# Kernel tuning notes

Hardware: AMD Instinct MI355X
Metric: run time of the kernel (lower is better)

Reference implementation:

```python
import jax, jax.numpy as jnp
import numpy as np

X = 2048      # hidden units per layer
Z = 4         # number of hidden layers
IN = 512      # input_dim
OUT = 256     # output_dim
B = 64        # batch
T = 128       # time steps
KEEP = 0.7    # Bernoulli keep prob y
RES = [0, 0, 1, 2]  # residual_in (first two unused by the branch structure)
NFUN = 5      # number of candidate transfer functions


def setup_inputs() -> dict:
    key = jax.random.key(0)
    ks = jax.random.split(key, 12)
    f32 = jnp.float32
    x = jax.random.normal(ks[0], (B, T, IN), f32)
    W_in = jax.random.normal(ks[1], (X, IN), f32) * jax.random.bernoulli(ks[2], KEEP, (X, IN)).astype(f32)
    b_in = jax.random.normal(ks[3], (X,), f32)
    W_h = jax.random.normal(ks[4], (Z, X, 2 * X), f32)
    # lateral inhibition block: hidden layer 1, second-half columns, zero diagonal
    lat = jax.random.normal(ks[5], (X, X), f32) * (1.0 - jnp.eye(X, dtype=f32))
    W_h = W_h.at[1, :, X:].set(lat)
    W_h = W_h * jax.random.bernoulli(ks[6], KEEP, (Z, X, 2 * X)).astype(f32)
    b_h = jax.random.normal(ks[7], (Z, X), f32)
    W_out = jax.random.normal(ks[8], (OUT, X), f32) * jax.random.bernoulli(ks[9], KEEP, (OUT, X)).astype(f32)
    b_out = jax.random.normal(ks[10], (OUT,), f32)
    act_ids = jax.random.randint(ks[11], (Z + 1, X), 0, NFUN)
    out_act_ids = jax.random.randint(jax.random.fold_in(key, 99), (OUT,), 0, NFUN)
    return dict(x=x, W_in=W_in, b_in=b_in, W_h=W_h, b_h=b_h,
                W_out=W_out, b_out=b_out, act_ids=act_ids, out_act_ids=out_act_ids)


def _rand_act(h, ids):
    # per-column random nonlinearity: ids [D] in {relu, sigmoid, tanh, leaky_relu(0.1), selu}
    stk = jnp.stack([
        jax.nn.relu(h),
        jax.nn.sigmoid(h),
        jnp.tanh(h),
        jnp.where(h >= 0, h, 0.1 * h),
        jax.nn.selu(h),
    ], axis=0)  # [5, B, D]
    oh = jax.nn.one_hot(ids, NFUN, dtype=h.dtype)  # [D, 5]
    return jnp.einsum('fbd,df->bd', stk, oh)


def _l2norm(v, eps=1e-12):
    # torch F.normalize along dim=1
    return v / jnp.maximum(jnp.linalg.norm(v, axis=1, keepdims=True), eps)


def reference(x, W_in, b_in, W_h, b_h, W_out, b_out, act_ids, out_act_ids):
    batch = x.shape[0]

    def step(carry, xt):
        bp, li = carry  # backprojection state, lateral inhibition state
        h0 = _rand_act(xt @ W_in.T + b_in, act_ids[0])
        h1 = _rand_act(jnp.concatenate([h0, bp], axis=-1) @ W_h[0].T + b_h[0], act_ids[1])
        h2 = _rand_act(jnp.concatenate([h1, li], axis=-1) @ W_h[1].T + b_h[1], act_ids[2])
        li_new = _l2norm(h2)
        outs = [h0, h1, h2]
        for i in range(2, Z):
            hin = jnp.concatenate([outs[i], outs[RES[i]]], axis=-1)
            outs.append(_rand_act(hin @ W_h[i].T + b_h[i], act_ids[i + 1]))
        bp_new = _l2norm(outs[-1])
        yt = _rand_act(outs[-1] @ W_out.T + b_out, out_act_ids)
        return (bp_new, li_new), yt

    init = (jnp.zeros((batch, X), x.dtype), jnp.zeros((batch, X), x.dtype))
    _, ys = jax.lax.scan(step, init, jnp.swapaxes(x, 0, 1))  # scan over time
    return jnp.swapaxes(ys, 0, 1)  # [B, T, OUT]
```

## Files before the change

### kernel.cpp

```cpp
#include <hip/hip_runtime.h>
#include <stdint.h>


typedef __bf16 bf16;
typedef __attribute__((ext_vector_type(8))) __bf16 bf16x8;
typedef __attribute__((ext_vector_type(4))) float f32x4;

#define BATCH 64
#define TSTEPS 128
#define INDIM 512
#define XDIM 2048
#define OUTDIM 256
#define SLOTE ((size_t)BATCH * XDIM)
#define NBLOCKS 256
#define GSTRIDE 64
#define PBPAR ((size_t)3 * BATCH * XDIM)

__device__ __forceinline__ float apply_act(float h, int id) {
  switch (id) {
    case 0: return fmaxf(h, 0.0f);
    case 1: return 1.0f / (1.0f + __expf(-h));
    case 2: return tanhf(h);
    case 3: return h >= 0.0f ? h : 0.1f * h;
    default: {
      const float sc = 1.0507009873554805f;
      const float al = 1.6732632423543772f;
      return h > 0.0f ? sc * h : sc * al * (__expf(h) - 1.0f);
    }
  }
}

__device__ __forceinline__ bf16x8 cload(const bf16* p) {
  union { unsigned long long q[2]; bf16x8 v; } u;
  const unsigned long long* qp = (const unsigned long long*)p;
  u.q[0] = __hip_atomic_load(qp, __ATOMIC_RELAXED, __HIP_MEMORY_SCOPE_AGENT);
  u.q[1] = __hip_atomic_load(qp + 1, __ATOMIC_RELAXED, __HIP_MEMORY_SCOPE_AGENT);
  return u.v;
}

__device__ __forceinline__ void cstore8(unsigned long long* p,
                                        unsigned long long v) {
  unsigned long long old = __hip_atomic_exchange(p, v, __ATOMIC_RELAXED,
                                                 __HIP_MEMORY_SCOPE_AGENT);
  asm volatile("" :: "v"(old));
}

__device__ __forceinline__ unsigned long long cload8(
    const unsigned long long* p) {
  return __hip_atomic_load(p, __ATOMIC_RELAXED, __HIP_MEMORY_SCOPE_AGENT);
}

__device__ __forceinline__ void phase_wait(unsigned* bars, int bid,
                                           unsigned ph) {
  if (threadIdx.x == 0) {
    unsigned* done = bars + (size_t)8 * GSTRIDE;
    unsigned* rel = bars + (size_t)(9 + (bid >> 5)) * GSTRIDE;
    if ((bid & 31) == 0) {
      while (__hip_atomic_load(done, __ATOMIC_RELAXED,
                               __HIP_MEMORY_SCOPE_AGENT) < 64u * ph) {
        __builtin_amdgcn_s_sleep(2);
      }
      __hip_atomic_fetch_add(rel, 1u, __ATOMIC_RELAXED,
                             __HIP_MEMORY_SCOPE_AGENT);
    } else {
      while (__hip_atomic_load(rel, __ATOMIC_RELAXED,
                               __HIP_MEMORY_SCOPE_AGENT) < ph) {
        __builtin_amdgcn_s_sleep(2);
      }
    }
  }
  __syncthreads();
}

template <bool SCALE_A2, bool EMIT_SS, bool PLAIN_A1>
__device__ __forceinline__ void layer_phase(
    const int tid, const int nt, const int kq,
    const bf16* __restrict__ A1, const bf16* __restrict__ A2,
    const bf16x8 (&wf)[2][4], const float* __restrict__ bias,
    const int* __restrict__ acts, const float* __restrict__ ss_in,
    float* __restrict__ ss_out, bf16* __restrict__ outb,
    float* __restrict__ pbuf, unsigned* __restrict__ flags,
    unsigned* __restrict__ bars, const unsigned ph,
    float (&red)[8][64][33]) {
  const int lane = tid & 63;
  const int w = tid >> 6;
  const int l15 = lane & 15;
  const int kb8 = (lane >> 4) * 8;
  const int q4 = lane >> 4;

  const bf16* As = (kq >= 2) ? A2 : A1;
  const int koff = (kq & 1) * 1024 + w * 128;
  const bf16* ap = As + (size_t)l15 * 2048 + koff + kb8;

  f32x4 acc[4][2];
  const f32x4 zero = {0.f, 0.f, 0.f, 0.f};
#pragma unroll
  for (int mt = 0; mt < 4; mt++) {
    acc[mt][0] = zero;
    acc[mt][1] = zero;
  }

  const bool plain = PLAIN_A1 && (kq < 2);
#pragma unroll
  for (int ks = 0; ks < 4; ks++) {
#pragma unroll
    for (int mt = 0; mt < 4; mt++) {
      const bf16* aptr = ap + (size_t)mt * 16 * 2048 + ks * 32;
      bf16x8 a = plain ? *(const bf16x8*)aptr : cload(aptr);
      acc[mt][0] = __builtin_amdgcn_mfma_f32_16x16x32_bf16(a, wf[0][ks], acc[mt][0], 0, 0, 0);
      acc[mt][1] = __builtin_amdgcn_mfma_f32_16x16x32_bf16(a, wf[1][ks], acc[mt][1], 0, 0, 0);
    }
  }

#pragma unroll
  for (int mt = 0; mt < 4; mt++)
#pragma unroll
    for (int n2 = 0; n2 < 2; n2++)
#pragma unroll
      for (int r = 0; r < 4; r++)
        red[w][mt * 16 + q4 * 4 + r][n2 * 16 + l15] = acc[mt][n2][r];
  __syncthreads();

  const int row = tid >> 3;
  const int c4 = (tid & 7) * 4;
  float v[4];
#pragma unroll
  for (int j = 0; j < 4; j++) {
    float s = 0.f;
#pragma unroll
    for (int ww = 0; ww < 8; ww++) s += red[ww][row][c4 + j];
    v[j] = s;
  }

  float* pbase = pbuf + (size_t)(ph & 1) * PBPAR;
  const size_t pidx = ((size_t)row) * XDIM + nt * 32 + c4;
  if (kq != 0) {
    float* pb = pbase + (size_t)(kq - 1) * BATCH * XDIM + pidx;
    union { float f[2]; unsigned long long u; } pk;
    pk.f[0] = v[0]; pk.f[1] = v[1];
    cstore8((unsigned long long*)pb, pk.u);
    pk.f[0] = v[2]; pk.f[1] = v[3];
    cstore8((unsigned long long*)(pb + 2), pk.u);
    __syncthreads();
    if (tid == 0) {
      __hip_atomic_fetch_add(flags + (size_t)nt * GSTRIDE, 1u,
                             __ATOMIC_RELAXED, __HIP_MEMORY_SCOPE_AGENT);
    }
  } else {
    if (tid == 0) {
      while (__hip_atomic_load(flags + (size_t)nt * GSTRIDE, __ATOMIC_RELAXED,
                               __HIP_MEMORY_SCOPE_AGENT) < 3u * ph) {
        __builtin_amdgcn_s_sleep(1);
      }
    }
    __syncthreads();
    float p1[4], p2[4], p3[4];
#pragma unroll
    for (int h = 0; h < 2; h++) {
      union { unsigned long long u; float f[2]; } u1, u2, u3;
      const unsigned long long* b1 =
          (const unsigned long long*)(pbase + pidx) + h;
      u1.u = cload8(b1);
      u2.u = cload8(b1 + (size_t)BATCH * XDIM / 2);
      u3.u = cload8(b1 + (size_t)BATCH * XDIM);
      p1[h * 2] = u1.f[0]; p1[h * 2 + 1] = u1.f[1];
      p2[h * 2] = u2.f[0]; p2[h * 2 + 1] = u2.f[1];
      p3[h * 2] = u3.f[0]; p3[h * 2 + 1] = u3.f[1];
    }
    float scale = 1.0f;
    if (SCALE_A2) {
      float ssv = __hip_atomic_load(ss_in + row, __ATOMIC_RELAXED,
                                    __HIP_MEMORY_SCOPE_AGENT);
      scale = 1.0f / fmaxf(sqrtf(ssv), 1e-12f);
    }
    const int cg = nt * 32 + c4;
    union { bf16 b[4]; unsigned long long u; } hk;
    float ssl = 0.f;
#pragma unroll
    for (int j = 0; j < 4; j++) {
      float lo = v[j] + p1[j];
      float hi = p2[j] + p3[j];
      float pre = (SCALE_A2 ? (lo + scale * hi) : (lo + hi)) + bias[cg + j];
      float av = apply_act(pre, acts[cg + j]);
      hk.b[j] = (bf16)av;
      ssl += av * av;
    }
    if (EMIT_SS) {
      ssl += __shfl_xor(ssl, 1);
      ssl += __shfl_xor(ssl, 2);
      ssl += __shfl_xor(ssl, 4);
      if ((tid & 7) == 0) atomicAdd(ss_out + row, ssl);
    }
    cstore8((unsigned long long*)(outb + (size_t)row * XDIM + cg), hk.u);
    __syncthreads();
    if (tid == 0) {
      __hip_atomic_fetch_add(bars + (size_t)8 * GSTRIDE, 1u, __ATOMIC_RELAXED,
                             __HIP_MEMORY_SCOPE_AGENT);
    }
  }
}

struct StepParams {
  bf16* h0;
  bf16* extra;
  bf16* h1;
  bf16* h2a;
  bf16* h2b;
  bf16* h3;
  const bf16* whb;
  const float* b_h;
  const int* acts;
  float* ss_li;
  float* ss_bp;
  float* pbuf;
  unsigned* flags;
  unsigned* bar;
};

__global__ __launch_bounds__(512, 2) void step_loop(StepParams p) {
  __shared__ float red[8][64][33];
  const int tid = threadIdx.x;
  const int bid = blockIdx.x;
  const int nt = bid & 63;
  const int kq = bid >> 6;
  const int lane = tid & 63;
  const int w = tid >> 6;
  const int l15 = lane & 15;
  const int kb8 = (lane >> 4) * 8;
  const size_t wstr = (size_t)XDIM * 2 * XDIM;

  const bf16* wb = p.whb + (size_t)(nt * 32 + l15) * 4096 + kq * 1024 +
                   w * 128 + kb8;
  bf16x8 wf0[2][4], wf1[2][4], wf2[2][4], wf3[2][4];
#pragma unroll
  for (int n2 = 0; n2 < 2; n2++) {
#pragma unroll
    for (int ks = 0; ks < 4; ks++) {
      const bf16* q = wb + (size_t)n2 * 16 * 4096 + ks * 32;
      wf0[n2][ks] = *(const bf16x8*)q;
      wf1[n2][ks] = *(const bf16x8*)(q + wstr);
      wf2[n2][ks] = *(const bf16x8*)(q + 2 * wstr);
      wf3[n2][ks] = *(const bf16x8*)(q + 3 * wstr);
    }
  }

  unsigned ph = 0;
  for (int t = 0; t < TSTEPS; t++) {
#pragma unroll
    for (int n2 = 0; n2 < 2; n2++)
#pragma unroll
      for (int ks = 0; ks < 4; ks++) {
        asm volatile("" : "+v"(wf0[n2][ks]), "+v"(wf1[n2][ks]),
                          "+v"(wf2[n2][ks]), "+v"(wf3[n2][ks]));
      }

    const bf16* h4t = (t < 2) ? p.extra + (size_t)t * SLOTE
                              : p.h0 + (size_t)(t - 2) * SLOTE;
    bf16* h4n = (t + 1 < 2) ? p.extra + (size_t)(t + 1) * SLOTE
                            : p.h0 + (size_t)(t - 1) * SLOTE;
    bf16* h2n = (t & 1) ? p.h2b : p.h2a;
    const bf16* h2o = (t & 1) ? p.h2a : p.h2b;

    ++ph;
    layer_phase<true, false, true>(tid, nt, kq, p.h0 + (size_t)t * SLOTE, h4t,
                                   wf0, p.b_h, p.acts + XDIM,
                                   p.ss_bp + t * BATCH, nullptr, p.h1,
                                   p.pbuf, p.flags, p.bar, ph, red);
    phase_wait(p.bar, bid, ph);

    ++ph;
    layer_phase<true, true, false>(tid, nt, kq, p.h1, h2o, wf1, p.b_h + XDIM,
                                   p.acts + 2 * XDIM, p.ss_li + t * BATCH,
                                   p.ss_li + (t + 1) * BATCH, h2n,
                                   p.pbuf, p.flags, p.bar, ph, red);
    phase_wait(p.bar, bid, ph);

    ++ph;
    layer_phase<false, false, false>(tid, nt, kq, h2n, p.h1, wf2,
                                     p.b_h + 2 * XDIM, p.acts + 3 * XDIM,
                                     nullptr, nullptr, p.h3,
                                     p.pbuf, p.flags, p.bar, ph, red);
    phase_wait(p.bar, bid, ph);

    ++ph;
    layer_phase<false, true, false>(tid, nt, kq, p.h3, h2n, wf3,
                                    p.b_h + 3 * XDIM, p.acts + 4 * XDIM,
                                    nullptr, p.ss_bp + (t + 1) * BATCH, h4n,
                                    p.pbuf, p.flags, p.bar, ph, red);
    phase_wait(p.bar, bid, ph);
  }
}

__global__ __launch_bounds__(256) void h0_gemm(
    const bf16* __restrict__ A, const bf16* __restrict__ W,
    const float* __restrict__ bias, const int* __restrict__ acts,
    bf16* __restrict__ outp) {
  const int tid = threadIdx.x;
  const int lane = tid & 63;
  const int wv = tid >> 6;
  const int wm = (wv & 1) * 32;
  const int wn = (wv >> 1) * 64;
  const int nblk = blockIdx.x * 128;
  const int mblk = blockIdx.y * 64;
  const int l15 = lane & 15;
  const int kb8 = (lane >> 4) * 8;

  f32x4 acc[2][4];
  const f32x4 zero = {0.f, 0.f, 0.f, 0.f};
#pragma unroll
  for (int i = 0; i < 2; i++)
#pragma unroll
    for (int j = 0; j < 4; j++) acc[i][j] = zero;

  for (int kt = 0; kt < INDIM; kt += 32) {
    bf16x8 a[2], b[4];
#pragma unroll
    for (int mt = 0; mt < 2; mt++) {
      int m = mblk + wm + mt * 16 + l15;
      a[mt] = *(const bf16x8*)(A + (size_t)m * INDIM + kt + kb8);
    }
#pragma unroll
    for (int nt = 0; nt < 4; nt++) {
      int n = nblk + wn + nt * 16 + l15;
      b[nt] = *(const bf16x8*)(W + (size_t)n * INDIM + kt + kb8);
    }
#pragma unroll
    for (int mt = 0; mt < 2; mt++)
#pragma unroll
      for (int nt = 0; nt < 4; nt++)
        acc[mt][nt] = __builtin_amdgcn_mfma_f32_16x16x32_bf16(a[mt], b[nt], acc[mt][nt], 0, 0, 0);
  }

#pragma unroll
  for (int mt = 0; mt < 2; mt++) {
#pragma unroll
    for (int nt = 0; nt < 4; nt++) {
      int n = nblk + wn + nt * 16 + l15;
      float bv = bias[n];
      int aid = acts[n];
#pragma unroll
      for (int rr = 0; rr < 4; rr++) {
        int m = wm + mt * 16 + (lane >> 4) * 4 + rr;
        float v = apply_act(acc[mt][nt][rr] + bv, aid);
        int rowg = mblk + m;
        int bb = rowg >> 7;
        int tt = rowg & 127;
        outp[((size_t)tt * BATCH + bb) * XDIM + n] = (bf16)v;
      }
    }
  }
}

__global__ __launch_bounds__(256) void ybat_gemm(
    const bf16* __restrict__ extra, const bf16* __restrict__ h0,
    const bf16* __restrict__ Wout, const float* __restrict__ bout,
    const int* __restrict__ oact, float* __restrict__ out) {
  const int t = blockIdx.y;
  const int s = t + 1;
  const bf16* A = (s < 2) ? (extra + (size_t)s * SLOTE)
                          : (h0 + (size_t)(s - 2) * SLOTE);
  const int tid = threadIdx.x;
  const int lane = tid & 63;
  const int wv = tid >> 6;
  const int wm = (wv & 1) * 32;
  const int wn = (wv >> 1) * 64;
  const int nblk = blockIdx.x * 128;
  const int l15 = lane & 15;
  const int kb8 = (lane >> 4) * 8;

  f32x4 acc[2][4];
  const f32x4 zero = {0.f, 0.f, 0.f, 0.f};
#pragma unroll
  for (int i = 0; i < 2; i++)
#pragma unroll
    for (int j = 0; j < 4; j++) acc[i][j] = zero;

  for (int kt = 0; kt < XDIM; kt += 32) {
    bf16x8 a[2], b[4];
#pragma unroll
    for (int mt = 0; mt < 2; mt++) {
      int m = wm + mt * 16 + l15;
      a[mt] = *(const bf16x8*)(A + (size_t)m * XDIM + kt + kb8);
    }
#pragma unroll
    for (int nt = 0; nt < 4; nt++) {
      int n = nblk + wn + nt * 16 + l15;
      b[nt] = *(const bf16x8*)(Wout + (size_t)n * XDIM + kt + kb8);
    }
#pragma unroll
    for (int mt = 0; mt < 2; mt++)
#pragma unroll
      for (int nt = 0; nt < 4; nt++)
        acc[mt][nt] = __builtin_amdgcn_mfma_f32_16x16x32_bf16(a[mt], b[nt], acc[mt][nt], 0, 0, 0);
  }

#pragma unroll
  for (int mt = 0; mt < 2; mt++) {
#pragma unroll
    for (int nt = 0; nt < 4; nt++) {
      int n = nblk + wn + nt * 16 + l15;
      float bv = bout[n];
      int aid = oact[n];
#pragma unroll
      for (int rr = 0; rr < 4; rr++) {
        int b = wm + mt * 16 + (lane >> 4) * 4 + rr;
        float v = apply_act(acc[mt][nt][rr] + bv, aid);
        out[((size_t)b * TSTEPS + t) * OUTDIM + n] = v;
      }
    }
  }
}

__global__ __launch_bounds__(256) void cvt_bf16(
    const float* __restrict__ in, bf16* __restrict__ out, int n4) {
  int i = blockIdx.x * 256 + threadIdx.x;
  if (i < n4) {
    float4 v = ((const float4*)in)[i];
    union { bf16 b[4]; unsigned long long u; } pk;
    pk.b[0] = (bf16)v.x;
    pk.b[1] = (bf16)v.y;
    pk.b[2] = (bf16)v.z;
    pk.b[3] = (bf16)v.w;
    ((unsigned long long*)out)[i] = pk.u;
  }
}

__global__ __launch_bounds__(256) void zero32(uint32_t* __restrict__ p, int n) {
  int i = blockIdx.x * 256 + threadIdx.x;
  if (i < n) p[i] = 0u;
}

extern "C" void kernel_launch(void* const* d_in, const int* in_sizes, int n_in,
                              void* d_out, int out_size, void* d_ws, size_t ws_size,
                              hipStream_t stream) {
  const float* x     = (const float*)d_in[0];
  const float* W_in  = (const float*)d_in[1];
  const float* b_in  = (const float*)d_in[2];
  const float* W_h   = (const float*)d_in[3];
  const float* b_h   = (const float*)d_in[4];
  const float* W_out = (const float*)d_in[5];
  const float* b_out = (const float*)d_in[6];
  const int* act_ids = (const int*)d_in[7];
  const int* out_act = (const int*)d_in[8];
  float* out = (float*)d_out;

  char* w = (char*)d_ws;
  bf16* xbf   = (bf16*)w; w += (size_t)BATCH * TSTEPS * INDIM * 2;
  bf16* winb  = (bf16*)w; w += (size_t)XDIM * INDIM * 2;
  bf16* whb   = (bf16*)w; w += (size_t)4 * XDIM * (2 * XDIM) * 2;
  bf16* woutb = (bf16*)w; w += (size_t)OUTDIM * XDIM * 2;
  bf16* h0    = (bf16*)w; w += (size_t)TSTEPS * SLOTE * 2;
  bf16* h1    = (bf16*)w; w += SLOTE * 2;
  bf16* h3    = (bf16*)w; w += SLOTE * 2;
  float* pbuf = (float*)w; w += (size_t)2 * PBPAR * 4;
  char* zstart = w;
  bf16* extra = (bf16*)w; w += 2 * SLOTE * 2;
  bf16* h2a   = (bf16*)w; w += SLOTE * 2;
  bf16* h2b   = (bf16*)w; w += SLOTE * 2;
  float* ss_li = (float*)w; w += (size_t)(TSTEPS + 1) * BATCH * 4;
  float* ss_bp = (float*)w; w += (size_t)(TSTEPS + 1) * BATCH * 4;
  unsigned* flags = (unsigned*)w; w += (size_t)64 * GSTRIDE * 4;
  unsigned* bar = (unsigned*)w; w += (size_t)32 * GSTRIDE * 4;
  int zero_u32 = (int)((w - zstart) / 4);

  cvt_bf16<<<4096, 256, 0, stream>>>(x, xbf, (BATCH * TSTEPS * INDIM) / 4);
  cvt_bf16<<<1024, 256, 0, stream>>>(W_in, winb, (XDIM * INDIM) / 4);
  cvt_bf16<<<32768, 256, 0, stream>>>(W_h, whb, (4 * XDIM * 2 * XDIM) / 4);
  cvt_bf16<<<512, 256, 0, stream>>>(W_out, woutb, (OUTDIM * XDIM) / 4);
  zero32<<<(zero_u32 + 255) / 256, 256, 0, stream>>>((uint32_t*)zstart, zero_u32);
  h0_gemm<<<dim3(16, 128), 256, 0, stream>>>(xbf, winb, b_in, act_ids, h0);

  StepParams sp;
  sp.h0 = h0;
  sp.extra = extra;
  sp.h1 = h1;
  sp.h2a = h2a;
  sp.h2b = h2b;
  sp.h3 = h3;
  sp.whb = whb;
  sp.b_h = b_h;
  sp.acts = act_ids;
  sp.ss_li = ss_li;
  sp.ss_bp = ss_bp;
  sp.pbuf = pbuf;
  sp.flags = flags;
  sp.bar = bar;
  void* kp[] = {&sp};
  (void)hipLaunchCooperativeKernel((const void*)step_loop, dim3(NBLOCKS),
                                   dim3(512), kp, 0, stream);

  ybat_gemm<<<dim3(2, TSTEPS), 256, 0, stream>>>(
      extra, h0, woutb, b_out, out_act, out);
}
```

Before: 8.597 ms.

## Relax grid barrier so residual-half blocks start before previous layer finishes

Moves the grid barrier from after each layer to before it, and lets blocks whose K-quarter reads only the second (older) input start one phase early, since that input was produced two phases back. Split-K completion flags become per-quarter counters instead of one shared atomic. The block-to-tile mapping is reordered so the four K-quarters of an output tile are adjacent block ids. This aims to cut barrier stall and atomic contention, at the cost of subtler ordering: it depends on the early-start blocks not reading or overwriting data still in use, including partial buffers that alternate by phase parity.

```diff
diff --git a/kernel.cpp b/kernel.cpp
--- a/kernel.cpp
+++ b/kernel.cpp
@@ -50,21 +50,21 @@
   return __hip_atomic_load(p, __ATOMIC_RELAXED, __HIP_MEMORY_SCOPE_AGENT);
 }
 
-__device__ __forceinline__ void phase_wait(unsigned* bars, int bid,
-                                           unsigned ph) {
+__device__ __forceinline__ void start_wait(unsigned* bars, int bid,
+                                           unsigned tgt) {
   if (threadIdx.x == 0) {
     unsigned* done = bars + (size_t)8 * GSTRIDE;
     unsigned* rel = bars + (size_t)(9 + (bid >> 5)) * GSTRIDE;
     if ((bid & 31) == 0) {
       while (__hip_atomic_load(done, __ATOMIC_RELAXED,
-                               __HIP_MEMORY_SCOPE_AGENT) < 64u * ph) {
+                               __HIP_MEMORY_SCOPE_AGENT) < 64u * (tgt - 1u)) {
         __builtin_amdgcn_s_sleep(2);
       }
       __hip_atomic_fetch_add(rel, 1u, __ATOMIC_RELAXED,
                              __HIP_MEMORY_SCOPE_AGENT);
     } else {
       while (__hip_atomic_load(rel, __ATOMIC_RELAXED,
-                               __HIP_MEMORY_SCOPE_AGENT) < ph) {
+                               __HIP_MEMORY_SCOPE_AGENT) < tgt) {
         __builtin_amdgcn_s_sleep(2);
       }
     }
@@ -143,13 +143,22 @@
     cstore8((unsigned long long*)(pb + 2), pk.u);
     __syncthreads();
     if (tid == 0) {
-      __hip_atomic_fetch_add(flags + (size_t)nt * GSTRIDE, 1u,
+      __hip_atomic_fetch_add(flags + (size_t)nt * GSTRIDE + kq, 1u,
                              __ATOMIC_RELAXED, __HIP_MEMORY_SCOPE_AGENT);
     }
   } else {
     if (tid == 0) {
-      while (__hip_atomic_load(flags + (size_t)nt * GSTRIDE, __ATOMIC_RELAXED,
-                               __HIP_MEMORY_SCOPE_AGENT) < 3u * ph) {
+      unsigned* f = flags + (size_t)nt * GSTRIDE;
+      while (__hip_atomic_load(f + 1, __ATOMIC_RELAXED,
+                               __HIP_MEMORY_SCOPE_AGENT) < ph) {
+        __builtin_amdgcn_s_sleep(1);
+      }
+      while (__hip_atomic_load(f + 2, __ATOMIC_RELAXED,
+                               __HIP_MEMORY_SCOPE_AGENT) < ph) {
+        __builtin_amdgcn_s_sleep(1);
+      }
+      while (__hip_atomic_load(f + 3, __ATOMIC_RELAXED,
+                               __HIP_MEMORY_SCOPE_AGENT) < ph) {
         __builtin_amdgcn_s_sleep(1);
       }
     }
@@ -221,8 +230,8 @@
   __shared__ float red[8][64][33];
   const int tid = threadIdx.x;
   const int bid = blockIdx.x;
-  const int nt = bid & 63;
-  const int kq = bid >> 6;
+  const int kq = bid & 3;
+  const int nt = bid >> 2;
   const int lane = tid & 63;
   const int w = tid >> 6;
   const int l15 = lane & 15;
@@ -244,6 +253,7 @@
     }
   }
 
+  const bool a2side = (kq >= 2);
   unsigned ph = 0;
   for (int t = 0; t < TSTEPS; t++) {
 #pragma unroll
@@ -262,32 +272,32 @@
     const bf16* h2o = (t & 1) ? p.h2a : p.h2b;
 
     ++ph;
+    start_wait(p.bar, bid, ph);
     layer_phase<true, false, true>(tid, nt, kq, p.h0 + (size_t)t * SLOTE, h4t,
                                    wf0, p.b_h, p.acts + XDIM,
                                    p.ss_bp + t * BATCH, nullptr, p.h1,
                                    p.pbuf, p.flags, p.bar, ph, red);
-    phase_wait(p.bar, bid, ph);
 
     ++ph;
+    start_wait(p.bar, bid, a2side ? ph - 1 : ph);
     layer_phase<true, true, false>(tid, nt, kq, p.h1, h2o, wf1, p.b_h + XDIM,
                                    p.acts + 2 * XDIM, p.ss_li + t * BATCH,
                                    p.ss_li + (t + 1) * BATCH, h2n,
                                    p.pbuf, p.flags, p.bar, ph, red);
-    phase_wait(p.bar, bid, ph);
 
     ++ph;
+    start_wait(p.bar, bid, a2side ? ph - 1 : ph);
     layer_phase<false, false, false>(tid, nt, kq, h2n, p.h1, wf2,
                                      p.b_h + 2 * XDIM, p.acts + 3 * XDIM,
                                      nullptr, nullptr, p.h3,
                                      p.pbuf, p.flags, p.bar, ph, red);
-    phase_wait(p.bar, bid, ph);
 
     ++ph;
+    start_wait(p.bar, bid, a2side ? ph - 1 : ph);
     layer_phase<false, true, false>(tid, nt, kq, p.h3, h2n, wf3,
                                     p.b_h + 3 * XDIM, p.acts + 4 * XDIM,
                                     nullptr, p.ss_bp + (t + 1) * BATCH, h4n,
                                     p.pbuf, p.flags, p.bar, ph, red);
-    phase_wait(p.bar, bid, ph);
   }
 }
 
```

After: 9.421 ms. 9.6% more time.
